# Optimization experiments

Hardware: AMD Instinct MI355X
Metric: run time of the kernel (lower is better)

The kernel has to match this reference:

```python
import jax, jax.numpy as jnp
import numpy as np

N = 100000      # nodes
E = 640000      # directed edges (before self-loops)
F_IN = 128      # num_features
C1 = 64         # latent_size (conv1 out, heads=1)
C2 = 16         # num_classes (conv2 out, heads=1)
NEG_SLOPE = 0.2


def setup_inputs() -> dict:
    key = jax.random.key(0)
    ks = jax.random.split(key, 10)
    s = 0.1
    return {
        "x": jax.random.normal(ks[0], (N, F_IN), jnp.float32),
        "edge_index": jax.random.randint(ks[1], (2, E), 0, N, dtype=jnp.int32),
        "W1": jax.random.normal(ks[2], (F_IN, C1), jnp.float32) * s,
        "att_src1": jax.random.normal(ks[3], (C1,), jnp.float32) * s,
        "att_dst1": jax.random.normal(ks[4], (C1,), jnp.float32) * s,
        "b1": jax.random.normal(ks[5], (C1,), jnp.float32) * s,
        "W2": jax.random.normal(ks[6], (C1, C2), jnp.float32) * s,
        "att_src2": jax.random.normal(ks[7], (C2,), jnp.float32) * s,
        "att_dst2": jax.random.normal(ks[8], (C2,), jnp.float32) * s,
        "b2": jax.random.normal(ks[9], (C2,), jnp.float32) * s,
    }


def gat_layer(x, src, dst, W, a_src, a_dst, b, n_nodes):
    # x: [N, F] -> h: [N, C] (heads=1)
    h = x @ W
    # per-edge attention logits: alpha_j + alpha_i, then leaky_relu
    alpha = jax.nn.leaky_relu((h @ a_src)[src] + (h @ a_dst)[dst], NEG_SLOPE)
    # scatter-softmax over destination-node groups (numerically stable)
    amax = jax.ops.segment_max(alpha, dst, num_segments=n_nodes)
    e = jnp.exp(alpha - amax[dst])
    denom = jax.ops.segment_sum(e, dst, num_segments=n_nodes)
    w = e / (denom[dst] + 1e-16)
    # gather src features, weight, scatter-add to dst
    out = jax.ops.segment_sum(h[src] * w[:, None], dst, num_segments=n_nodes)
    return out + b


def kl_to_std_normal(out):
    # GIB reparameterize: mean = out[:, :ceil(C/2)], std = softplus(out[:, -ceil(C/2):])
    size = (out.shape[-1] + 1) // 2
    mean = out[:, :size]
    std = jax.nn.softplus(out[:, -size:]) + 1e-10
    kl = -jnp.log(std) + 0.5 * (std * std + mean * mean - 1.0)
    return kl.reshape(out.shape[0], -1, 1)  # [N, size, heads=1]


def reference(x, edge_index, W1, att_src1, att_dst1, b1, W2, att_src2, att_dst2, b2):
    n = x.shape[0]
    loop = jnp.arange(n, dtype=edge_index.dtype)  # PyG GATConv add_self_loops=True
    src = jnp.concatenate([edge_index[0], loop])
    dst = jnp.concatenate([edge_index[1], loop])

    out1 = gat_layer(x, src, dst, W1, att_src1, att_dst1, b1, n)
    ixz1 = kl_to_std_normal(out1)

    h = jax.nn.elu(out1)  # dropout is a no-op in eval mode
    out2 = gat_layer(h, src, dst, W2, att_src2, att_dst2, b2, n)
    ixz2 = kl_to_std_normal(out2)

    return (out2, ixz1, ixz2)
```

## Files before the change

kernel.cpp:

```cpp
#include <hip/hip_runtime.h>
#include <math.h>

#define NN 100000
#define NE 640000
#define FIN 128
#define C1 64
#define C2 16
#define NEG_SLOPE 0.2f
#define SLOTS 32
#define G1_BLOCKS ((NN + 127) / 128)
#define SORT_EPB 2048
#define SORT_NBLK ((NE + SORT_EPB - 1) / SORT_EPB)
#define NBUCK 512
#define NBUCK_USED ((NN + 255) / 256)

typedef unsigned int uint32;
typedef __attribute__((ext_vector_type(8))) short bf16x8;
typedef __attribute__((ext_vector_type(4))) float f32x4;

static __device__ __forceinline__ float lrelu(float x) { return x > 0.f ? x : NEG_SLOPE * x; }
static __device__ __forceinline__ float softplusn(float x) {
    return fmaxf(x, 0.f) + __logf(1.f + __expf(-fabsf(x)));
}
static __device__ __forceinline__ unsigned short f2bf(float f) {
    uint32 u = __float_as_uint(f);
    u += 0x7fffu + ((u >> 16) & 1u);
    return (unsigned short)(u >> 16);
}
static __device__ __forceinline__ float bf2f_lo(uint32 p) { return __uint_as_float(p << 16); }
static __device__ __forceinline__ float bf2f_hi(uint32 p) { return __uint_as_float(p & 0xffff0000u); }

#define G1T 2
__global__ __launch_bounds__(256, 3) void k_g1hist(
        const float* __restrict__ x, const float* __restrict__ W1,
        const float* __restrict__ attS, const float* __restrict__ attD,
        unsigned short* __restrict__ h1b, float* __restrict__ as1, float* __restrict__ ad1,
        const int* __restrict__ ei, int* __restrict__ blockHist) {
    __shared__ uint32 ts[4][16][36];
    __shared__ int lh[NBUCK];
    if (blockIdx.x >= G1_BLOCKS) {
        int blk = (int)blockIdx.x - G1_BLOCKS;
        int t = threadIdx.x;
        for (int i = t; i < NBUCK; i += 256) lh[i] = 0;
        __syncthreads();
        int base = blk * SORT_EPB;
#pragma unroll
        for (int k = 0; k < 8; k++) {
            int e = base + k * 256 + t;
            if (e < NE) atomicAdd(&lh[ei[NE + e] >> 8], 1);
        }
        __syncthreads();
        for (int i = t; i < NBUCK; i += 256) blockHist[i * SORT_NBLK + blk] = lh[i];
        return;
    }
    int lane = threadIdx.x & 63;
    int wv = threadIdx.x >> 6;
    int col = lane & 15;
    int g = lane >> 4;
    int wbase = (blockIdx.x * 4 + wv) * (G1T * 16);
    if (wbase >= NN) return;

    bf16x8 bfr[4][4];
#pragma unroll
    for (int t = 0; t < 4; t++)
#pragma unroll
        for (int j = 0; j < 4; j++) {
            int c = col + j * 16;
#pragma unroll
            for (int i = 0; i < 8; i++)
                bfr[t][j][i] = (short)f2bf(W1[(t * 32 + g * 8 + i) * C1 + c]);
        }
    float ats[4], atd[4];
#pragma unroll
    for (int j = 0; j < 4; j++) { ats[j] = attS[col + j * 16]; atd[j] = attD[col + j * 16]; }

    for (int tl = 0; tl < G1T; tl++) {
        int tbase = wbase + tl * 16;
        int arow = tbase + col; if (arow > NN - 1) arow = NN - 1;
        const float* xr = &x[(size_t)arow * FIN];
        float4 f0[4], f1[4];
#pragma unroll
        for (int t = 0; t < 4; t++) {
            f0[t] = *reinterpret_cast<const float4*>(&xr[t * 32 + g * 8]);
            f1[t] = *reinterpret_cast<const float4*>(&xr[t * 32 + g * 8 + 4]);
        }
        bf16x8 a[4];
#pragma unroll
        for (int t = 0; t < 4; t++) {
            a[t][0] = (short)f2bf(f0[t].x); a[t][1] = (short)f2bf(f0[t].y);
            a[t][2] = (short)f2bf(f0[t].z); a[t][3] = (short)f2bf(f0[t].w);
            a[t][4] = (short)f2bf(f1[t].x); a[t][5] = (short)f2bf(f1[t].y);
            a[t][6] = (short)f2bf(f1[t].z); a[t][7] = (short)f2bf(f1[t].w);
        }
        f32x4 acc[4];
#pragma unroll
        for (int j = 0; j < 4; j++) acc[j] = (f32x4){0.f, 0.f, 0.f, 0.f};
#pragma unroll
        for (int t = 0; t < 4; t++)
#pragma unroll
            for (int j = 0; j < 4; j++)
                acc[j] = __builtin_amdgcn_mfma_f32_16x16x32_bf16(a[t], bfr[t][j], acc[j], 0, 0, 0);

        float sA[4] = {0.f, 0.f, 0.f, 0.f}, sD[4] = {0.f, 0.f, 0.f, 0.f};
        unsigned short* tsw = (unsigned short*)&ts[wv][0][0];
#pragma unroll
        for (int reg = 0; reg < 4; reg++) {
            int trow = g * 4 + reg;
#pragma unroll
            for (int j = 0; j < 4; j++) {
                float v = acc[j][reg];
                tsw[trow * 72 + col + j * 16] = f2bf(v);
                sA[reg] = fmaf(v, ats[j], sA[reg]);
                sD[reg] = fmaf(v, atd[j], sD[reg]);
            }
        }
        __builtin_amdgcn_wave_barrier();
        {
            int rrow = lane >> 2, rq = lane & 3;
            uint4 w0 = *reinterpret_cast<const uint4*>(&ts[wv][rrow][rq * 8]);
            uint4 w1 = *reinterpret_cast<const uint4*>(&ts[wv][rrow][rq * 8 + 4]);
            int orow = tbase + rrow;
            if (orow < NN) {
                unsigned short* op = &h1b[(size_t)orow * C1 + rq * 16];
                *reinterpret_cast<uint4*>(op) = w0;
                *reinterpret_cast<uint4*>(op + 8) = w1;
            }
        }
        __builtin_amdgcn_wave_barrier();
#pragma unroll
        for (int off = 8; off; off >>= 1)
#pragma unroll
            for (int reg = 0; reg < 4; reg++) {
                sA[reg] += __shfl_xor(sA[reg], off);
                sD[reg] += __shfl_xor(sD[reg], off);
            }
        if (col == 0) {
#pragma unroll
            for (int reg = 0; reg < 4; reg++) {
                int row = tbase + g * 4 + reg;
                if (row < NN) { as1[row] = sA[reg]; ad1[row] = sD[reg]; }
            }
        }
    }
}

__global__ __launch_bounds__(256) void k_scan(int* __restrict__ blockHist, int* __restrict__ bucketCnt) {
    __shared__ int s[SORT_NBLK];
    int b = blockIdx.x, t = threadIdx.x;
    for (int i = t; i < SORT_NBLK; i += 256) s[i] = blockHist[b * SORT_NBLK + i];
    __syncthreads();
    for (int d = 1; d < SORT_NBLK; d <<= 1) {
        int i0 = t, i1 = t + 256;
        int v0 = 0, v1 = 0;
        if (i0 >= d && i0 < SORT_NBLK) v0 = s[i0 - d];
        if (i1 >= d && i1 < SORT_NBLK) v1 = s[i1 - d];
        __syncthreads();
        if (i0 >= d && i0 < SORT_NBLK) s[i0] += v0;
        if (i1 >= d && i1 < SORT_NBLK) s[i1] += v1;
        __syncthreads();
    }
    for (int i = t; i < SORT_NBLK; i += 256)
        blockHist[b * SORT_NBLK + i] = (i == 0) ? 0 : s[i - 1];
    if (t == 0) bucketCnt[b] = s[SORT_NBLK - 1];
}

__global__ __launch_bounds__(256) void k_scat1(const int* __restrict__ ei,
        const int* __restrict__ blockHist, uint32* __restrict__ ebuf) {
    __shared__ int lh[NBUCK];
    int t = threadIdx.x;
    for (int i = t; i < NBUCK; i += 256) lh[i] = blockHist[i * SORT_NBLK + blockIdx.x];
    __syncthreads();
    int base = blockIdx.x * SORT_EPB;
#pragma unroll
    for (int k = 0; k < 8; k++) {
        int e = base + k * 256 + t;
        if (e < NE) {
            int src = ei[e], dst = ei[NE + e];
            int bin = dst >> 8;
            int pos = atomicAdd(&lh[bin], 1);
            ebuf[bin * SORT_EPB + pos] = ((uint32)src << 8) | (uint32)(dst & 255);
        }
    }
}

__global__ __launch_bounds__(256, 4) void k_agg1(
        const uint32* __restrict__ ebuf, const int* __restrict__ bucketCnt,
        const float* __restrict__ as1, const float* __restrict__ ad1,
        const unsigned short* __restrict__ h1b, const float* __restrict__ b1,
        unsigned short* __restrict__ heb, float* __restrict__ ixz1) {
    __shared__ int lcnt[256];
    __shared__ int lcsr[256 * SLOTS];
    int t = threadIdx.x, b = blockIdx.x;
    lcnt[t] = 0;
    for (int i = t; i < 256 * SLOTS; i += 256) lcsr[i] = 0;
    __syncthreads();
    int n = bucketCnt[b]; if (n > SORT_EPB) n = SORT_EPB;
    for (int i = t; i < n; i += 256) {
        uint32 e = ebuf[b * SORT_EPB + i];
        int ln = (int)(e & 255u);
        int pos = atomicAdd(&lcnt[ln], 1);
        if (pos < SLOTS) lcsr[ln * SLOTS + pos] = (int)(e >> 8);
    }
    __syncthreads();
    int lane = t & 63, wv = t >> 6;
    int grp = lane >> 4, gl = lane & 15;
    int gbase = grp << 4;
    for (int it = 0; it < 16; it++) {
        int ln = it * 16 + wv * 4 + grp;
        int node = b * 256 + ln;
        if (node >= NN) continue;
        int dcnt = lcnt[ln];
        int s_l = lcsr[ln * SLOTS + gl];
        int4 S0 = *reinterpret_cast<const int4*>(&lcsr[ln * SLOTS]);
        int4 S1 = *reinterpret_cast<const int4*>(&lcsr[ln * SLOTS + 4]);
        int4 S2 = *reinterpret_cast<const int4*>(&lcsr[ln * SLOTS + 8]);
        int4 S3 = *reinterpret_cast<const int4*>(&lcsr[ln * SLOTS + 12]);
        float adn = ad1[node];
        float asn = as1[node];
        float asv = as1[s_l];
        float4 o;
        if (dcnt <= 16) {
            float al = (gl < dcnt) ? lrelu(asv + adn) : -1e30f;
            float wl = __expf(al);
            float den = wl;
#pragma unroll
            for (int off = 8; off; off >>= 1) den += __shfl_xor(den, off);
            float wself = __expf(lrelu(asn + adn));
            den += wself;
            float inv = __builtin_amdgcn_rcpf(den + 1e-16f);
            wl *= inv; wself *= inv;
            const unsigned short* hb = h1b + gl * 4;
            uint2 PS  = *reinterpret_cast<const uint2*>(&hb[(size_t)node * C1]);
            uint2 P0  = *reinterpret_cast<const uint2*>(&hb[(size_t)S0.x * C1]);
            uint2 P1  = *reinterpret_cast<const uint2*>(&hb[(size_t)S0.y * C1]);
            uint2 P2  = *reinterpret_cast<const uint2*>(&hb[(size_t)S0.z * C1]);
            uint2 P3  = *reinterpret_cast<const uint2*>(&hb[(size_t)S0.w * C1]);
            uint2 P4  = *reinterpret_cast<const uint2*>(&hb[(size_t)S1.x * C1]);
            uint2 P5  = *reinterpret_cast<const uint2*>(&hb[(size_t)S1.y * C1]);
            uint2 P6  = *reinterpret_cast<const uint2*>(&hb[(size_t)S1.z * C1]);
            uint2 P7  = *reinterpret_cast<const uint2*>(&hb[(size_t)S1.w * C1]);
            uint2 P8  = *reinterpret_cast<const uint2*>(&hb[(size_t)S2.x * C1]);
            uint2 P9  = *reinterpret_cast<const uint2*>(&hb[(size_t)S2.y * C1]);
            uint2 P10 = *reinterpret_cast<const uint2*>(&hb[(size_t)S2.z * C1]);
            uint2 P11 = *reinterpret_cast<const uint2*>(&hb[(size_t)S2.w * C1]);
            uint2 P12 = *reinterpret_cast<const uint2*>(&hb[(size_t)S3.x * C1]);
            uint2 P13 = *reinterpret_cast<const uint2*>(&hb[(size_t)S3.y * C1]);
            uint2 P14 = *reinterpret_cast<const uint2*>(&hb[(size_t)S3.z * C1]);
            uint2 P15 = *reinterpret_cast<const uint2*>(&hb[(size_t)S3.w * C1]);
            float4 acc;
            acc.x = wself * bf2f_lo(PS.x);
            acc.y = wself * bf2f_hi(PS.x);
            acc.z = wself * bf2f_lo(PS.y);
            acc.w = wself * bf2f_hi(PS.y);
#define ACC1(k, Pk) { float w = __shfl(wl, gbase | k); \
            acc.x = fmaf(w, bf2f_lo(Pk.x), acc.x); acc.y = fmaf(w, bf2f_hi(Pk.x), acc.y); \
            acc.z = fmaf(w, bf2f_lo(Pk.y), acc.z); acc.w = fmaf(w, bf2f_hi(Pk.y), acc.w); }
            ACC1(0, P0)  ACC1(1, P1)  ACC1(2, P2)  ACC1(3, P3)
            ACC1(4, P4)  ACC1(5, P5)  ACC1(6, P6)  ACC1(7, P7)
            ACC1(8, P8)  ACC1(9, P9)  ACC1(10, P10) ACC1(11, P11)
            ACC1(12, P12) ACC1(13, P13) ACC1(14, P14) ACC1(15, P15)
#undef ACC1
            o = acc;
        } else {
            int dcl = dcnt < SLOTS ? dcnt : SLOTS;
            float aself = lrelu(asn + adn);
            float m = aself;
            for (int e = gl; e < dcl; e += 16) m = fmaxf(m, lrelu(as1[lcsr[ln * SLOTS + e]] + adn));
#pragma unroll
            for (int off = 8; off; off >>= 1) m = fmaxf(m, __shfl_xor(m, off));
            float den = 0.f;
            for (int e = gl; e < dcl; e += 16) den += __expf(lrelu(as1[lcsr[ln * SLOTS + e]] + adn) - m);
#pragma unroll
            for (int off = 8; off; off >>= 1) den += __shfl_xor(den, off);
            den += __expf(aself - m);
            float inv = __builtin_amdgcn_rcpf(den + 1e-16f);
            float wsf = __expf(aself - m) * inv;
            uint2 ps = *reinterpret_cast<const uint2*>(&h1b[(size_t)node * C1 + gl * 4]);
            float4 acc;
            acc.x = wsf * bf2f_lo(ps.x);
            acc.y = wsf * bf2f_hi(ps.x);
            acc.z = wsf * bf2f_lo(ps.y);
            acc.w = wsf * bf2f_hi(ps.y);
            for (int e = 0; e < dcl; e++) {
                int s = lcsr[ln * SLOTS + e];
                float wgt = __expf(lrelu(as1[s] + adn) - m) * inv;
                uint2 p = *reinterpret_cast<const uint2*>(&h1b[(size_t)s * C1 + gl * 4]);
                acc.x = fmaf(wgt, bf2f_lo(p.x), acc.x);
                acc.y = fmaf(wgt, bf2f_hi(p.x), acc.y);
                acc.z = fmaf(wgt, bf2f_lo(p.y), acc.z);
                acc.w = fmaf(wgt, bf2f_hi(p.y), acc.w);
            }
            o = acc;
        }
        float4 bv = *reinterpret_cast<const float4*>(&b1[gl * 4]);
        o.x += bv.x; o.y += bv.y; o.z += bv.z; o.w += bv.w;
        float4 he;
        he.x = o.x > 0.f ? o.x : __expf(o.x) - 1.f;
        he.y = o.y > 0.f ? o.y : __expf(o.y) - 1.f;
        he.z = o.z > 0.f ? o.z : __expf(o.z) - 1.f;
        he.w = o.w > 0.f ? o.w : __expf(o.w) - 1.f;
        uint2 hw;
        hw.x = (uint32)f2bf(he.x) | ((uint32)f2bf(he.y) << 16);
        hw.y = (uint32)f2bf(he.z) | ((uint32)f2bf(he.w) << 16);
        *reinterpret_cast<uint2*>(&heb[(size_t)node * C1 + gl * 4]) = hw;
        float4 oth;
        oth.x = __shfl_down(o.x, 8);
        oth.y = __shfl_down(o.y, 8);
        oth.z = __shfl_down(o.z, 8);
        oth.w = __shfl_down(o.w, 8);
        if (gl < 8) {
            float4 kl; float sd;
            sd = softplusn(oth.x) + 1e-10f; kl.x = -__logf(sd) + 0.5f * (sd * sd + o.x * o.x - 1.f);
            sd = softplusn(oth.y) + 1e-10f; kl.y = -__logf(sd) + 0.5f * (sd * sd + o.y * o.y - 1.f);
            sd = softplusn(oth.z) + 1e-10f; kl.z = -__logf(sd) + 0.5f * (sd * sd + o.z * o.z - 1.f);
            sd = softplusn(oth.w) + 1e-10f; kl.w = -__logf(sd) + 0.5f * (sd * sd + o.w * o.w - 1.f);
            *reinterpret_cast<float4*>(&ixz1[(size_t)node * 32 + gl * 4]) = kl;
        }
    }
}

#define G2T 4
__global__ __launch_bounds__(256, 4) void k_gemm2(
        const unsigned short* __restrict__ heb, const float* __restrict__ W2,
        const float* __restrict__ attS, const float* __restrict__ attD,
        unsigned short* __restrict__ h2b, float* __restrict__ as2, float* __restrict__ ad2) {
    int lane = threadIdx.x & 63;
    int wv = threadIdx.x >> 6;
    int col = lane & 15, g = lane >> 4;
    int wbase = (blockIdx.x * 4 + wv) * (G2T * 16);
    if (wbase >= NN) return;
    bf16x8 bfr[2];
#pragma unroll
    for (int t = 0; t < 2; t++)
#pragma unroll
        for (int i = 0; i < 8; i++)
            bfr[t][i] = (short)f2bf(W2[(t * 32 + g * 8 + i) * C2 + col]);
    float ats = attS[col], atd = attD[col];
#pragma unroll
    for (int tl = 0; tl < G2T; tl++) {
        int tbase = wbase + tl * 16;
        if (tbase >= NN) break;
        int arow = tbase + col; if (arow > NN - 1) arow = NN - 1;
        bf16x8 a0 = *reinterpret_cast<const bf16x8*>(&heb[(size_t)arow * C1 + g * 8]);
        bf16x8 a1 = *reinterpret_cast<const bf16x8*>(&heb[(size_t)arow * C1 + 32 + g * 8]);
        f32x4 acc = (f32x4){0.f, 0.f, 0.f, 0.f};
        acc = __builtin_amdgcn_mfma_f32_16x16x32_bf16(a0, bfr[0], acc, 0, 0, 0);
        acc = __builtin_amdgcn_mfma_f32_16x16x32_bf16(a1, bfr[1], acc, 0, 0, 0);
        float sA[4], sD[4];
#pragma unroll
        for (int reg = 0; reg < 4; reg++) {
            int row = tbase + g * 4 + reg;
            if (row < NN) h2b[(size_t)row * C2 + col] = f2bf(acc[reg]);
            sA[reg] = acc[reg] * ats;
            sD[reg] = acc[reg] * atd;
        }
#pragma unroll
        for (int off = 8; off; off >>= 1)
#pragma unroll
            for (int reg = 0; reg < 4; reg++) {
                sA[reg] += __shfl_xor(sA[reg], off);
                sD[reg] += __shfl_xor(sD[reg], off);
            }
        if (col == 0) {
#pragma unroll
            for (int reg = 0; reg < 4; reg++) {
                int row = tbase + g * 4 + reg;
                if (row < NN) { as2[row] = sA[reg]; ad2[row] = sD[reg]; }
            }
        }
    }
}

__global__ __launch_bounds__(256, 4) void k_agg2(
        const uint32* __restrict__ ebuf, const int* __restrict__ bucketCnt,
        const float* __restrict__ as2, const float* __restrict__ ad2,
        const unsigned short* __restrict__ h2b, const float* __restrict__ b2,
        float* __restrict__ out2, float* __restrict__ ixz2) {
    __shared__ int lcnt[256];
    __shared__ int lcsr[256 * SLOTS];
    int t = threadIdx.x, b = blockIdx.x;
    lcnt[t] = 0;
    for (int i = t; i < 256 * SLOTS; i += 256) lcsr[i] = 0;
    __syncthreads();
    int n = bucketCnt[b]; if (n > SORT_EPB) n = SORT_EPB;
    for (int i = t; i < n; i += 256) {
        uint32 e = ebuf[b * SORT_EPB + i];
        int ln = (int)(e & 255u);
        int pos = atomicAdd(&lcnt[ln], 1);
        if (pos < SLOTS) lcsr[ln * SLOTS + pos] = (int)(e >> 8);
    }
    __syncthreads();
    int lane = t & 63, wv = t >> 6;
    int grp = lane >> 4, gl = lane & 15;
    int gbase = grp << 4;
    int f4 = gl & 3, eg = gl >> 2;
    for (int it = 0; it < 16; it++) {
        int ln = it * 16 + wv * 4 + grp;
        int node = b * 256 + ln;
        if (node >= NN) continue;
        int dcnt = lcnt[ln];
        int s_l = lcsr[ln * SLOTS + gl];
        int sk0 = lcsr[ln * SLOTS + eg];
        int sk1 = lcsr[ln * SLOTS + 4 + eg];
        int sk2 = lcsr[ln * SLOTS + 8 + eg];
        int sk3 = lcsr[ln * SLOTS + 12 + eg];
        float adn = ad2[node];
        float asn = as2[node];
        float asv = as2[s_l];
        float out;
        if (dcnt <= 16) {
            float al = (gl < dcnt) ? lrelu(asv + adn) : -1e30f;
            float wl = __expf(al);
            float den = wl;
#pragma unroll
            for (int off = 8; off; off >>= 1) den += __shfl_xor(den, off);
            float wself = __expf(lrelu(asn + adn));
            den += wself;
            float inv = __builtin_amdgcn_rcpf(den + 1e-16f);
            wl *= inv; wself *= inv;
            uint2 PS = *reinterpret_cast<const uint2*>(&h2b[(size_t)node * C2 + f4 * 4]);
            uint2 P0 = *reinterpret_cast<const uint2*>(&h2b[(size_t)sk0 * C2 + f4 * 4]);
            uint2 P1 = *reinterpret_cast<const uint2*>(&h2b[(size_t)sk1 * C2 + f4 * 4]);
            uint2 P2 = *reinterpret_cast<const uint2*>(&h2b[(size_t)sk2 * C2 + f4 * 4]);
            uint2 P3 = *reinterpret_cast<const uint2*>(&h2b[(size_t)sk3 * C2 + f4 * 4]);
            float ws = (eg == 0) ? wself : 0.f;
            float4 acc;
            acc.x = ws * bf2f_lo(PS.x);
            acc.y = ws * bf2f_hi(PS.x);
            acc.z = ws * bf2f_lo(PS.y);
            acc.w = ws * bf2f_hi(PS.y);
            float w0 = __shfl(wl, gbase | eg);
            float w1 = __shfl(wl, gbase | (4 + eg));
            float w2 = __shfl(wl, gbase | (8 + eg));
            float w3 = __shfl(wl, gbase | (12 + eg));
            acc.x = fmaf(w0, bf2f_lo(P0.x), acc.x);
            acc.y = fmaf(w0, bf2f_hi(P0.x), acc.y);
            acc.z = fmaf(w0, bf2f_lo(P0.y), acc.z);
            acc.w = fmaf(w0, bf2f_hi(P0.y), acc.w);
            acc.x = fmaf(w1, bf2f_lo(P1.x), acc.x);
            acc.y = fmaf(w1, bf2f_hi(P1.x), acc.y);
            acc.z = fmaf(w1, bf2f_lo(P1.y), acc.z);
            acc.w = fmaf(w1, bf2f_hi(P1.y), acc.w);
            acc.x = fmaf(w2, bf2f_lo(P2.x), acc.x);
            acc.y = fmaf(w2, bf2f_hi(P2.x), acc.y);
            acc.z = fmaf(w2, bf2f_lo(P2.y), acc.z);
            acc.w = fmaf(w2, bf2f_hi(P2.y), acc.w);
            acc.x = fmaf(w3, bf2f_lo(P3.x), acc.x);
            acc.y = fmaf(w3, bf2f_hi(P3.x), acc.y);
            acc.z = fmaf(w3, bf2f_lo(P3.y), acc.z);
            acc.w = fmaf(w3, bf2f_hi(P3.y), acc.w);
#pragma unroll
            for (int off = 4; off <= 8; off <<= 1) {
                acc.x += __shfl_xor(acc.x, off);
                acc.y += __shfl_xor(acc.y, off);
                acc.z += __shfl_xor(acc.z, off);
                acc.w += __shfl_xor(acc.w, off);
            }
            int srcl = gbase | (gl >> 2);
            float t0 = __shfl(acc.x, srcl);
            float t1 = __shfl(acc.y, srcl);
            float t2 = __shfl(acc.z, srcl);
            float t3 = __shfl(acc.w, srcl);
            float t01 = (gl & 1) ? t1 : t0;
            float t23 = (gl & 1) ? t3 : t2;
            out = (gl & 2) ? t23 : t01;
        } else {
            int dcl = dcnt < SLOTS ? dcnt : SLOTS;
            float aself = lrelu(asn + adn);
            float m = aself;
            for (int e = gl; e < dcl; e += 16) m = fmaxf(m, lrelu(as2[lcsr[ln * SLOTS + e]] + adn));
#pragma unroll
            for (int off = 8; off; off >>= 1) m = fmaxf(m, __shfl_xor(m, off));
            float den = 0.f;
            for (int e = gl; e < dcl; e += 16) den += __expf(lrelu(as2[lcsr[ln * SLOTS + e]] + adn) - m);
#pragma unroll
            for (int off = 8; off; off >>= 1) den += __shfl_xor(den, off);
            den += __expf(aself - m);
            float inv = __builtin_amdgcn_rcpf(den + 1e-16f);
            float wsf = __expf(aself - m) * inv;
            float acc = wsf * __uint_as_float(((uint32)h2b[(size_t)node * C2 + gl]) << 16);
            for (int e = 0; e < dcl; e++) {
                int s = lcsr[ln * SLOTS + e];
                float wgt = __expf(lrelu(as2[s] + adn) - m) * inv;
                acc = fmaf(wgt, __uint_as_float(((uint32)h2b[(size_t)s * C2 + gl]) << 16), acc);
            }
            out = acc;
        }
        out += b2[gl];
        out2[(size_t)node * C2 + gl] = out;
        float other = __shfl_down(out, 8);
        if (gl < 8) {
            float sd = softplusn(other) + 1e-10f;
            float kl = -__logf(sd) + 0.5f * (sd * sd + out * out - 1.f);
            ixz2[(size_t)node * 8 + gl] = kl;
        }
    }
}

extern "C" void kernel_launch(void* const* d_in, const int* in_sizes, int n_in,
                              void* d_out, int out_size, void* d_ws, size_t ws_size,
                              hipStream_t stream) {
    const float* x     = (const float*)d_in[0];
    const int*   ei    = (const int*)d_in[1];
    const float* W1    = (const float*)d_in[2];
    const float* aS1   = (const float*)d_in[3];
    const float* aD1   = (const float*)d_in[4];
    const float* b1    = (const float*)d_in[5];
    const float* W2    = (const float*)d_in[6];
    const float* aS2   = (const float*)d_in[7];
    const float* aD2   = (const float*)d_in[8];
    const float* b2    = (const float*)d_in[9];

    float* out = (float*)d_out;
    float* out2 = out;
    float* ixz1 = out + (size_t)NN * C2;
    float* ixz2 = ixz1 + (size_t)NN * 32;

    char* p = (char*)d_ws;
    auto alloc = [&](size_t bytes) -> void* {
        void* r = (void*)p;
        p += (bytes + 255) & ~(size_t)255;
        return r;
    };
    int* blockHist  = (int*)alloc((size_t)NBUCK * SORT_NBLK * 4);
    int* bucketCnt  = (int*)alloc((size_t)NBUCK * 4);
    uint32* ebuf    = (uint32*)alloc((size_t)NBUCK * SORT_EPB * 4);
    unsigned short* h1b = (unsigned short*)alloc((size_t)NN * C1 * 2);
    float* as1   = (float*)alloc((size_t)NN * 4);
    float* ad1   = (float*)alloc((size_t)NN * 4);
    unsigned short* heb = (unsigned short*)alloc((size_t)NN * C1 * 2);
    unsigned short* h2b = (unsigned short*)alloc((size_t)NN * C2 * 2);
    float* as2   = (float*)alloc((size_t)NN * 4);
    float* ad2   = (float*)alloc((size_t)NN * 4);
    (void)ws_size; (void)in_sizes; (void)n_in; (void)out_size;

    k_g1hist<<<G1_BLOCKS + SORT_NBLK, 256, 0, stream>>>(x, W1, aS1, aD1, h1b, as1, ad1, ei, blockHist);

    k_scan <<<NBUCK, 256, 0, stream>>>(blockHist, bucketCnt);
    k_scat1<<<SORT_NBLK, 256, 0, stream>>>(ei, blockHist, ebuf);

    k_agg1<<<NBUCK_USED, 256, 0, stream>>>(ebuf, bucketCnt, as1, ad1, h1b, b1, heb, ixz1);

    k_gemm2<<<(NN + 4 * G2T * 16 - 1) / (4 * G2T * 16), 256, 0, stream>>>(heb, W2, aS2, aD2, h2b, as2, ad2);
    k_agg2<<<NBUCK_USED, 256, 0, stream>>>(ebuf, bucketCnt, as2, ad2, h2b, b2, out2, ixz2);
}
```

Measured before the change: 117.2 us.

## Shrink destination bins to 16 nodes so aggregation launches one block per bin

```diff
diff --git a/kernel.cpp b/kernel.cpp
--- a/kernel.cpp
+++ b/kernel.cpp
@@ -11,8 +11,8 @@
 #define G1_BLOCKS ((NN + 127) / 128)
 #define SORT_EPB 2048
 #define SORT_NBLK ((NE + SORT_EPB - 1) / SORT_EPB)
-#define NBUCK 512
-#define NBUCK_USED ((NN + 255) / 256)
+#define NBIN ((NN + 15) / 16)
+#define BINCAP 192
 
 typedef unsigned int uint32;
 typedef __attribute__((ext_vector_type(8))) short bf16x8;
@@ -37,20 +37,20 @@
         unsigned short* __restrict__ h1b, float* __restrict__ as1, float* __restrict__ ad1,
         const int* __restrict__ ei, int* __restrict__ blockHist) {
     __shared__ uint32 ts[4][16][36];
-    __shared__ int lh[NBUCK];
+    __shared__ int lh[NBIN];
     if (blockIdx.x >= G1_BLOCKS) {
         int blk = (int)blockIdx.x - G1_BLOCKS;
         int t = threadIdx.x;
-        for (int i = t; i < NBUCK; i += 256) lh[i] = 0;
+        for (int i = t; i < NBIN; i += 256) lh[i] = 0;
         __syncthreads();
         int base = blk * SORT_EPB;
 #pragma unroll
         for (int k = 0; k < 8; k++) {
             int e = base + k * 256 + t;
-            if (e < NE) atomicAdd(&lh[ei[NE + e] >> 8], 1);
+            if (e < NE) atomicAdd(&lh[ei[NE + e] >> 4], 1);
         }
         __syncthreads();
-        for (int i = t; i < NBUCK; i += 256) blockHist[i * SORT_NBLK + blk] = lh[i];
+        for (int i = t; i < NBIN; i += 256) blockHist[(size_t)i * SORT_NBLK + blk] = lh[i];
         return;
     }
     int lane = threadIdx.x & 63;
@@ -144,10 +144,10 @@
     }
 }
 
-__global__ __launch_bounds__(256) void k_scan(int* __restrict__ blockHist, int* __restrict__ bucketCnt) {
+__global__ __launch_bounds__(256) void k_scan(int* __restrict__ blockHist, int* __restrict__ binCnt) {
     __shared__ int s[SORT_NBLK];
     int b = blockIdx.x, t = threadIdx.x;
-    for (int i = t; i < SORT_NBLK; i += 256) s[i] = blockHist[b * SORT_NBLK + i];
+    for (int i = t; i < SORT_NBLK; i += 256) s[i] = blockHist[(size_t)b * SORT_NBLK + i];
     __syncthreads();
     for (int d = 1; d < SORT_NBLK; d <<= 1) {
         int i0 = t, i1 = t + 256;
@@ -160,15 +160,15 @@
         __syncthreads();
     }
     for (int i = t; i < SORT_NBLK; i += 256)
-        blockHist[b * SORT_NBLK + i] = (i == 0) ? 0 : s[i - 1];
-    if (t == 0) bucketCnt[b] = s[SORT_NBLK - 1];
+        blockHist[(size_t)b * SORT_NBLK + i] = (i == 0) ? 0 : s[i - 1];
+    if (t == 0) binCnt[b] = s[SORT_NBLK - 1];
 }
 
 __global__ __launch_bounds__(256) void k_scat1(const int* __restrict__ ei,
         const int* __restrict__ blockHist, uint32* __restrict__ ebuf) {
-    __shared__ int lh[NBUCK];
+    __shared__ int lh[NBIN];
     int t = threadIdx.x;
-    for (int i = t; i < NBUCK; i += 256) lh[i] = blockHist[i * SORT_NBLK + blockIdx.x];
+    for (int i = t; i < NBIN; i += 256) lh[i] = blockHist[(size_t)i * SORT_NBLK + blockIdx.x];
     __syncthreads();
     int base = blockIdx.x * SORT_EPB;
 #pragma unroll
@@ -176,146 +176,145 @@
         int e = base + k * 256 + t;
         if (e < NE) {
             int src = ei[e], dst = ei[NE + e];
-            int bin = dst >> 8;
+            int bin = dst >> 4;
             int pos = atomicAdd(&lh[bin], 1);
-            ebuf[bin * SORT_EPB + pos] = ((uint32)src << 8) | (uint32)(dst & 255);
+            if (pos < BINCAP)
+                ebuf[(size_t)bin * BINCAP + pos] = ((uint32)src << 4) | (uint32)(dst & 15);
         }
     }
 }
 
 __global__ __launch_bounds__(256, 4) void k_agg1(
-        const uint32* __restrict__ ebuf, const int* __restrict__ bucketCnt,
+        const uint32* __restrict__ ebuf, const int* __restrict__ binCnt,
         const float* __restrict__ as1, const float* __restrict__ ad1,
         const unsigned short* __restrict__ h1b, const float* __restrict__ b1,
         unsigned short* __restrict__ heb, float* __restrict__ ixz1) {
-    __shared__ int lcnt[256];
-    __shared__ int lcsr[256 * SLOTS];
+    __shared__ int lcnt[16];
+    __shared__ int lcsr[16 * SLOTS];
     int t = threadIdx.x, b = blockIdx.x;
-    lcnt[t] = 0;
-    for (int i = t; i < 256 * SLOTS; i += 256) lcsr[i] = 0;
+    if (t < 16) lcnt[t] = 0;
+    for (int i = t; i < 16 * SLOTS; i += 256) lcsr[i] = 0;
     __syncthreads();
-    int n = bucketCnt[b]; if (n > SORT_EPB) n = SORT_EPB;
-    for (int i = t; i < n; i += 256) {
-        uint32 e = ebuf[b * SORT_EPB + i];
-        int ln = (int)(e & 255u);
+    int n = binCnt[b]; if (n > BINCAP) n = BINCAP;
+    if (t < n) {
+        uint32 e = ebuf[(size_t)b * BINCAP + t];
+        int ln = (int)(e & 15u);
         int pos = atomicAdd(&lcnt[ln], 1);
-        if (pos < SLOTS) lcsr[ln * SLOTS + pos] = (int)(e >> 8);
+        if (pos < SLOTS) lcsr[ln * SLOTS + pos] = (int)(e >> 4);
     }
     __syncthreads();
     int lane = t & 63, wv = t >> 6;
     int grp = lane >> 4, gl = lane & 15;
     int gbase = grp << 4;
-    for (int it = 0; it < 16; it++) {
-        int ln = it * 16 + wv * 4 + grp;
-        int node = b * 256 + ln;
-        if (node >= NN) continue;
-        int dcnt = lcnt[ln];
-        int s_l = lcsr[ln * SLOTS + gl];
-        int4 S0 = *reinterpret_cast<const int4*>(&lcsr[ln * SLOTS]);
-        int4 S1 = *reinterpret_cast<const int4*>(&lcsr[ln * SLOTS + 4]);
-        int4 S2 = *reinterpret_cast<const int4*>(&lcsr[ln * SLOTS + 8]);
-        int4 S3 = *reinterpret_cast<const int4*>(&lcsr[ln * SLOTS + 12]);
-        float adn = ad1[node];
-        float asn = as1[node];
-        float asv = as1[s_l];
-        float4 o;
-        if (dcnt <= 16) {
-            float al = (gl < dcnt) ? lrelu(asv + adn) : -1e30f;
-            float wl = __expf(al);
-            float den = wl;
-#pragma unroll
-            for (int off = 8; off; off >>= 1) den += __shfl_xor(den, off);
-            float wself = __expf(lrelu(asn + adn));
-            den += wself;
-            float inv = __builtin_amdgcn_rcpf(den + 1e-16f);
-            wl *= inv; wself *= inv;
-            const unsigned short* hb = h1b + gl * 4;
-            uint2 PS  = *reinterpret_cast<const uint2*>(&hb[(size_t)node * C1]);
-            uint2 P0  = *reinterpret_cast<const uint2*>(&hb[(size_t)S0.x * C1]);
-            uint2 P1  = *reinterpret_cast<const uint2*>(&hb[(size_t)S0.y * C1]);
-            uint2 P2  = *reinterpret_cast<const uint2*>(&hb[(size_t)S0.z * C1]);
-            uint2 P3  = *reinterpret_cast<const uint2*>(&hb[(size_t)S0.w * C1]);
-            uint2 P4  = *reinterpret_cast<const uint2*>(&hb[(size_t)S1.x * C1]);
-            uint2 P5  = *reinterpret_cast<const uint2*>(&hb[(size_t)S1.y * C1]);
-            uint2 P6  = *reinterpret_cast<const uint2*>(&hb[(size_t)S1.z * C1]);
-            uint2 P7  = *reinterpret_cast<const uint2*>(&hb[(size_t)S1.w * C1]);
-            uint2 P8  = *reinterpret_cast<const uint2*>(&hb[(size_t)S2.x * C1]);
-            uint2 P9  = *reinterpret_cast<const uint2*>(&hb[(size_t)S2.y * C1]);
-            uint2 P10 = *reinterpret_cast<const uint2*>(&hb[(size_t)S2.z * C1]);
-            uint2 P11 = *reinterpret_cast<const uint2*>(&hb[(size_t)S2.w * C1]);
-            uint2 P12 = *reinterpret_cast<const uint2*>(&hb[(size_t)S3.x * C1]);
-            uint2 P13 = *reinterpret_cast<const uint2*>(&hb[(size_t)S3.y * C1]);
-            uint2 P14 = *reinterpret_cast<const uint2*>(&hb[(size_t)S3.z * C1]);
-            uint2 P15 = *reinterpret_cast<const uint2*>(&hb[(size_t)S3.w * C1]);
-            float4 acc;
-            acc.x = wself * bf2f_lo(PS.x);
-            acc.y = wself * bf2f_hi(PS.x);
-            acc.z = wself * bf2f_lo(PS.y);
-            acc.w = wself * bf2f_hi(PS.y);
+    int ln = wv * 4 + grp;
+    int node = b * 16 + ln;
+    if (node >= NN) return;
+    int dcnt = lcnt[ln];
+    int s_l = lcsr[ln * SLOTS + gl];
+    int4 S0 = *reinterpret_cast<const int4*>(&lcsr[ln * SLOTS]);
+    int4 S1 = *reinterpret_cast<const int4*>(&lcsr[ln * SLOTS + 4]);
+    int4 S2 = *reinterpret_cast<const int4*>(&lcsr[ln * SLOTS + 8]);
+    int4 S3 = *reinterpret_cast<const int4*>(&lcsr[ln * SLOTS + 12]);
+    float adn = ad1[node];
+    float asn = as1[node];
+    float asv = as1[s_l];
+    float4 o;
+    if (dcnt <= 16) {
+        float al = (gl < dcnt) ? lrelu(asv + adn) : -1e30f;
+        float wl = __expf(al);
+        float den = wl;
+#pragma unroll
+        for (int off = 8; off; off >>= 1) den += __shfl_xor(den, off);
+        float wself = __expf(lrelu(asn + adn));
+        den += wself;
+        float inv = __builtin_amdgcn_rcpf(den + 1e-16f);
+        wl *= inv; wself *= inv;
+        const unsigned short* hb = h1b + gl * 4;
+        uint2 PS  = *reinterpret_cast<const uint2*>(&hb[(size_t)node * C1]);
+        uint2 P0  = *reinterpret_cast<const uint2*>(&hb[(size_t)S0.x * C1]);
+        uint2 P1  = *reinterpret_cast<const uint2*>(&hb[(size_t)S0.y * C1]);
+        uint2 P2  = *reinterpret_cast<const uint2*>(&hb[(size_t)S0.z * C1]);
+        uint2 P3  = *reinterpret_cast<const uint2*>(&hb[(size_t)S0.w * C1]);
+        uint2 P4  = *reinterpret_cast<const uint2*>(&hb[(size_t)S1.x * C1]);
+        uint2 P5  = *reinterpret_cast<const uint2*>(&hb[(size_t)S1.y * C1]);
+        uint2 P6  = *reinterpret_cast<const uint2*>(&hb[(size_t)S1.z * C1]);
+        uint2 P7  = *reinterpret_cast<const uint2*>(&hb[(size_t)S1.w * C1]);
+        uint2 P8  = *reinterpret_cast<const uint2*>(&hb[(size_t)S2.x * C1]);
+        uint2 P9  = *reinterpret_cast<const uint2*>(&hb[(size_t)S2.y * C1]);
+        uint2 P10 = *reinterpret_cast<const uint2*>(&hb[(size_t)S2.z * C1]);
+        uint2 P11 = *reinterpret_cast<const uint2*>(&hb[(size_t)S2.w * C1]);
+        uint2 P12 = *reinterpret_cast<const uint2*>(&hb[(size_t)S3.x * C1]);
+        uint2 P13 = *reinterpret_cast<const uint2*>(&hb[(size_t)S3.y * C1]);
+        uint2 P14 = *reinterpret_cast<const uint2*>(&hb[(size_t)S3.z * C1]);
+        uint2 P15 = *reinterpret_cast<const uint2*>(&hb[(size_t)S3.w * C1]);
+        float4 acc;
+        acc.x = wself * bf2f_lo(PS.x);
+        acc.y = wself * bf2f_hi(PS.x);
+        acc.z = wself * bf2f_lo(PS.y);
+        acc.w = wself * bf2f_hi(PS.y);
 #define ACC1(k, Pk) { float w = __shfl(wl, gbase | k); \
-            acc.x = fmaf(w, bf2f_lo(Pk.x), acc.x); acc.y = fmaf(w, bf2f_hi(Pk.x), acc.y); \
-            acc.z = fmaf(w, bf2f_lo(Pk.y), acc.z); acc.w = fmaf(w, bf2f_hi(Pk.y), acc.w); }
-            ACC1(0, P0)  ACC1(1, P1)  ACC1(2, P2)  ACC1(3, P3)
-            ACC1(4, P4)  ACC1(5, P5)  ACC1(6, P6)  ACC1(7, P7)
-            ACC1(8, P8)  ACC1(9, P9)  ACC1(10, P10) ACC1(11, P11)
-            ACC1(12, P12) ACC1(13, P13) ACC1(14, P14) ACC1(15, P15)
+        acc.x = fmaf(w, bf2f_lo(Pk.x), acc.x); acc.y = fmaf(w, bf2f_hi(Pk.x), acc.y); \
+        acc.z = fmaf(w, bf2f_lo(Pk.y), acc.z); acc.w = fmaf(w, bf2f_hi(Pk.y), acc.w); }
+        ACC1(0, P0)  ACC1(1, P1)  ACC1(2, P2)  ACC1(3, P3)
+        ACC1(4, P4)  ACC1(5, P5)  ACC1(6, P6)  ACC1(7, P7)
+        ACC1(8, P8)  ACC1(9, P9)  ACC1(10, P10) ACC1(11, P11)
+        ACC1(12, P12) ACC1(13, P13) ACC1(14, P14) ACC1(15, P15)
 #undef ACC1
-            o = acc;
-        } else {
-            int dcl = dcnt < SLOTS ? dcnt : SLOTS;
-            float aself = lrelu(asn + adn);
-            float m = aself;
-            for (int e = gl; e < dcl; e += 16) m = fmaxf(m, lrelu(as1[lcsr[ln * SLOTS + e]] + adn));
-#pragma unroll
-            for (int off = 8; off; off >>= 1) m = fmaxf(m, __shfl_xor(m, off));
-            float den = 0.f;
-            for (int e = gl; e < dcl; e += 16) den += __expf(lrelu(as1[lcsr[ln * SLOTS + e]] + adn) - m);
-#pragma unroll
-            for (int off = 8; off; off >>= 1) den += __shfl_xor(den, off);
-            den += __expf(aself - m);
-            float inv = __builtin_amdgcn_rcpf(den + 1e-16f);
-            float wsf = __expf(aself - m) * inv;
-            uint2 ps = *reinterpret_cast<const uint2*>(&h1b[(size_t)node * C1 + gl * 4]);
-            float4 acc;
-            acc.x = wsf * bf2f_lo(ps.x);
-            acc.y = wsf * bf2f_hi(ps.x);
-            acc.z = wsf * bf2f_lo(ps.y);
-            acc.w = wsf * bf2f_hi(ps.y);
-            for (int e = 0; e < dcl; e++) {
-                int s = lcsr[ln * SLOTS + e];
-                float wgt = __expf(lrelu(as1[s] + adn) - m) * inv;
-                uint2 p = *reinterpret_cast<const uint2*>(&h1b[(size_t)s * C1 + gl * 4]);
-                acc.x = fmaf(wgt, bf2f_lo(p.x), acc.x);
-                acc.y = fmaf(wgt, bf2f_hi(p.x), acc.y);
-                acc.z = fmaf(wgt, bf2f_lo(p.y), acc.z);
-                acc.w = fmaf(wgt, bf2f_hi(p.y), acc.w);
-            }
-            o = acc;
-        }
-        float4 bv = *reinterpret_cast<const float4*>(&b1[gl * 4]);
-        o.x += bv.x; o.y += bv.y; o.z += bv.z; o.w += bv.w;
-        float4 he;
-        he.x = o.x > 0.f ? o.x : __expf(o.x) - 1.f;
-        he.y = o.y > 0.f ? o.y : __expf(o.y) - 1.f;
-        he.z = o.z > 0.f ? o.z : __expf(o.z) - 1.f;
-        he.w = o.w > 0.f ? o.w : __expf(o.w) - 1.f;
-        uint2 hw;
-        hw.x = (uint32)f2bf(he.x) | ((uint32)f2bf(he.y) << 16);
-        hw.y = (uint32)f2bf(he.z) | ((uint32)f2bf(he.w) << 16);
-        *reinterpret_cast<uint2*>(&heb[(size_t)node * C1 + gl * 4]) = hw;
-        float4 oth;
-        oth.x = __shfl_down(o.x, 8);
-        oth.y = __shfl_down(o.y, 8);
-        oth.z = __shfl_down(o.z, 8);
-        oth.w = __shfl_down(o.w, 8);
-        if (gl < 8) {
-            float4 kl; float sd;
-            sd = softplusn(oth.x) + 1e-10f; kl.x = -__logf(sd) + 0.5f * (sd * sd + o.x * o.x - 1.f);
-            sd = softplusn(oth.y) + 1e-10f; kl.y = -__logf(sd) + 0.5f * (sd * sd + o.y * o.y - 1.f);
-            sd = softplusn(oth.z) + 1e-10f; kl.z = -__logf(sd) + 0.5f * (sd * sd + o.z * o.z - 1.f);
-            sd = softplusn(oth.w) + 1e-10f; kl.w = -__logf(sd) + 0.5f * (sd * sd + o.w * o.w - 1.f);
-            *reinterpret_cast<float4*>(&ixz1[(size_t)node * 32 + gl * 4]) = kl;
-        }
+        o = acc;
+    } else {
+        int dcl = dcnt < SLOTS ? dcnt : SLOTS;
+        float aself = lrelu(asn + adn);
+        float m = aself;
+        for (int e = gl; e < dcl; e += 16) m = fmaxf(m, lrelu(as1[lcsr[ln * SLOTS + e]] + adn));
+#pragma unroll
+        for (int off = 8; off; off >>= 1) m = fmaxf(m, __shfl_xor(m, off));
+        float den = 0.f;
+        for (int e = gl; e < dcl; e += 16) den += __expf(lrelu(as1[lcsr[ln * SLOTS + e]] + adn) - m);
+#pragma unroll
+        for (int off = 8; off; off >>= 1) den += __shfl_xor(den, off);
+        den += __expf(aself - m);
+        float inv = __builtin_amdgcn_rcpf(den + 1e-16f);
+        float wsf = __expf(aself - m) * inv;
+        uint2 ps = *reinterpret_cast<const uint2*>(&h1b[(size_t)node * C1 + gl * 4]);
+        float4 acc;
+        acc.x = wsf * bf2f_lo(ps.x);
+        acc.y = wsf * bf2f_hi(ps.x);
+        acc.z = wsf * bf2f_lo(ps.y);
+        acc.w = wsf * bf2f_hi(ps.y);
+        for (int e = 0; e < dcl; e++) {
+            int s = lcsr[ln * SLOTS + e];
+            float wgt = __expf(lrelu(as1[s] + adn) - m) * inv;
+            uint2 p = *reinterpret_cast<const uint2*>(&h1b[(size_t)s * C1 + gl * 4]);
+            acc.x = fmaf(wgt, bf2f_lo(p.x), acc.x);
+            acc.y = fmaf(wgt, bf2f_hi(p.x), acc.y);
+            acc.z = fmaf(wgt, bf2f_lo(p.y), acc.z);
+            acc.w = fmaf(wgt, bf2f_hi(p.y), acc.w);
+        }
+        o = acc;
+    }
+    float4 bv = *reinterpret_cast<const float4*>(&b1[gl * 4]);
+    o.x += bv.x; o.y += bv.y; o.z += bv.z; o.w += bv.w;
+    float4 he;
+    he.x = o.x > 0.f ? o.x : __expf(o.x) - 1.f;
+    he.y = o.y > 0.f ? o.y : __expf(o.y) - 1.f;
+    he.z = o.z > 0.f ? o.z : __expf(o.z) - 1.f;
+    he.w = o.w > 0.f ? o.w : __expf(o.w) - 1.f;
+    uint2 hw;
+    hw.x = (uint32)f2bf(he.x) | ((uint32)f2bf(he.y) << 16);
+    hw.y = (uint32)f2bf(he.z) | ((uint32)f2bf(he.w) << 16);
+    *reinterpret_cast<uint2*>(&heb[(size_t)node * C1 + gl * 4]) = hw;
+    float4 oth;
+    oth.x = __shfl_down(o.x, 8);
+    oth.y = __shfl_down(o.y, 8);
+    oth.z = __shfl_down(o.z, 8);
+    oth.w = __shfl_down(o.w, 8);
+    if (gl < 8) {
+        float4 kl; float sd;
+        sd = softplusn(oth.x) + 1e-10f; kl.x = -__logf(sd) + 0.5f * (sd * sd + o.x * o.x - 1.f);
+        sd = softplusn(oth.y) + 1e-10f; kl.y = -__logf(sd) + 0.5f * (sd * sd + o.y * o.y - 1.f);
+        sd = softplusn(oth.z) + 1e-10f; kl.z = -__logf(sd) + 0.5f * (sd * sd + o.z * o.z - 1.f);
+        sd = softplusn(oth.w) + 1e-10f; kl.w = -__logf(sd) + 0.5f * (sd * sd + o.w * o.w - 1.f);
+        *reinterpret_cast<float4*>(&ixz1[(size_t)node * 32 + gl * 4]) = kl;
     }
 }
 
@@ -372,128 +371,126 @@
 }
 
 __global__ __launch_bounds__(256, 4) void k_agg2(
-        const uint32* __restrict__ ebuf, const int* __restrict__ bucketCnt,
+        const uint32* __restrict__ ebuf, const int* __restrict__ binCnt,
         const float* __restrict__ as2, const float* __restrict__ ad2,
         const unsigned short* __restrict__ h2b, const float* __restrict__ b2,
         float* __restrict__ out2, float* __restrict__ ixz2) {
-    __shared__ int lcnt[256];
-    __shared__ int lcsr[256 * SLOTS];
+    __shared__ int lcnt[16];
+    __shared__ int lcsr[16 * SLOTS];
     int t = threadIdx.x, b = blockIdx.x;
-    lcnt[t] = 0;
-    for (int i = t; i < 256 * SLOTS; i += 256) lcsr[i] = 0;
+    if (t < 16) lcnt[t] = 0;
+    for (int i = t; i < 16 * SLOTS; i += 256) lcsr[i] = 0;
     __syncthreads();
-    int n = bucketCnt[b]; if (n > SORT_EPB) n = SORT_EPB;
-    for (int i = t; i < n; i += 256) {
-        uint32 e = ebuf[b * SORT_EPB + i];
-        int ln = (int)(e & 255u);
+    int n = binCnt[b]; if (n > BINCAP) n = BINCAP;
+    if (t < n) {
+        uint32 e = ebuf[(size_t)b * BINCAP + t];
+        int ln = (int)(e & 15u);
         int pos = atomicAdd(&lcnt[ln], 1);
-        if (pos < SLOTS) lcsr[ln * SLOTS + pos] = (int)(e >> 8);
+        if (pos < SLOTS) lcsr[ln * SLOTS + pos] = (int)(e >> 4);
     }
     __syncthreads();
     int lane = t & 63, wv = t >> 6;
     int grp = lane >> 4, gl = lane & 15;
     int gbase = grp << 4;
     int f4 = gl & 3, eg = gl >> 2;
-    for (int it = 0; it < 16; it++) {
-        int ln = it * 16 + wv * 4 + grp;
-        int node = b * 256 + ln;
-        if (node >= NN) continue;
-        int dcnt = lcnt[ln];
-        int s_l = lcsr[ln * SLOTS + gl];
-        int sk0 = lcsr[ln * SLOTS + eg];
-        int sk1 = lcsr[ln * SLOTS + 4 + eg];
-        int sk2 = lcsr[ln * SLOTS + 8 + eg];
-        int sk3 = lcsr[ln * SLOTS + 12 + eg];
-        float adn = ad2[node];
-        float asn = as2[node];
-        float asv = as2[s_l];
-        float out;
-        if (dcnt <= 16) {
-            float al = (gl < dcnt) ? lrelu(asv + adn) : -1e30f;
-            float wl = __expf(al);
-            float den = wl;
-#pragma unroll
-            for (int off = 8; off; off >>= 1) den += __shfl_xor(den, off);
-            float wself = __expf(lrelu(asn + adn));
-            den += wself;
-            float inv = __builtin_amdgcn_rcpf(den + 1e-16f);
-            wl *= inv; wself *= inv;
-            uint2 PS = *reinterpret_cast<const uint2*>(&h2b[(size_t)node * C2 + f4 * 4]);
-            uint2 P0 = *reinterpret_cast<const uint2*>(&h2b[(size_t)sk0 * C2 + f4 * 4]);
-            uint2 P1 = *reinterpret_cast<const uint2*>(&h2b[(size_t)sk1 * C2 + f4 * 4]);
-            uint2 P2 = *reinterpret_cast<const uint2*>(&h2b[(size_t)sk2 * C2 + f4 * 4]);
-            uint2 P3 = *reinterpret_cast<const uint2*>(&h2b[(size_t)sk3 * C2 + f4 * 4]);
-            float ws = (eg == 0) ? wself : 0.f;
-            float4 acc;
-            acc.x = ws * bf2f_lo(PS.x);
-            acc.y = ws * bf2f_hi(PS.x);
-            acc.z = ws * bf2f_lo(PS.y);
-            acc.w = ws * bf2f_hi(PS.y);
-            float w0 = __shfl(wl, gbase | eg);
-            float w1 = __shfl(wl, gbase | (4 + eg));
-            float w2 = __shfl(wl, gbase | (8 + eg));
-            float w3 = __shfl(wl, gbase | (12 + eg));
-            acc.x = fmaf(w0, bf2f_lo(P0.x), acc.x);
-            acc.y = fmaf(w0, bf2f_hi(P0.x), acc.y);
-            acc.z = fmaf(w0, bf2f_lo(P0.y), acc.z);
-            acc.w = fmaf(w0, bf2f_hi(P0.y), acc.w);
-            acc.x = fmaf(w1, bf2f_lo(P1.x), acc.x);
-            acc.y = fmaf(w1, bf2f_hi(P1.x), acc.y);
-            acc.z = fmaf(w1, bf2f_lo(P1.y), acc.z);
-            acc.w = fmaf(w1, bf2f_hi(P1.y), acc.w);
-            acc.x = fmaf(w2, bf2f_lo(P2.x), acc.x);
-            acc.y = fmaf(w2, bf2f_hi(P2.x), acc.y);
-            acc.z = fmaf(w2, bf2f_lo(P2.y), acc.z);
-            acc.w = fmaf(w2, bf2f_hi(P2.y), acc.w);
-            acc.x = fmaf(w3, bf2f_lo(P3.x), acc.x);
-            acc.y = fmaf(w3, bf2f_hi(P3.x), acc.y);
-            acc.z = fmaf(w3, bf2f_lo(P3.y), acc.z);
-            acc.w = fmaf(w3, bf2f_hi(P3.y), acc.w);
-#pragma unroll
-            for (int off = 4; off <= 8; off <<= 1) {
-                acc.x += __shfl_xor(acc.x, off);
-                acc.y += __shfl_xor(acc.y, off);
-                acc.z += __shfl_xor(acc.z, off);
-                acc.w += __shfl_xor(acc.w, off);
-            }
-            int srcl = gbase | (gl >> 2);
-            float t0 = __shfl(acc.x, srcl);
-            float t1 = __shfl(acc.y, srcl);
-            float t2 = __shfl(acc.z, srcl);
-            float t3 = __shfl(acc.w, srcl);
-            float t01 = (gl & 1) ? t1 : t0;
-            float t23 = (gl & 1) ? t3 : t2;
-            out = (gl & 2) ? t23 : t01;
-        } else {
-            int dcl = dcnt < SLOTS ? dcnt : SLOTS;
-            float aself = lrelu(asn + adn);
-            float m = aself;
-            for (int e = gl; e < dcl; e += 16) m = fmaxf(m, lrelu(as2[lcsr[ln * SLOTS + e]] + adn));
-#pragma unroll
-            for (int off = 8; off; off >>= 1) m = fmaxf(m, __shfl_xor(m, off));
-            float den = 0.f;
-            for (int e = gl; e < dcl; e += 16) den += __expf(lrelu(as2[lcsr[ln * SLOTS + e]] + adn) - m);
-#pragma unroll
-            for (int off = 8; off; off >>= 1) den += __shfl_xor(den, off);
-            den += __expf(aself - m);
-            float inv = __builtin_amdgcn_rcpf(den + 1e-16f);
-            float wsf = __expf(aself - m) * inv;
-            float acc = wsf * __uint_as_float(((uint32)h2b[(size_t)node * C2 + gl]) << 16);
-            for (int e = 0; e < dcl; e++) {
-                int s = lcsr[ln * SLOTS + e];
-                float wgt = __expf(lrelu(as2[s] + adn) - m) * inv;
-                acc = fmaf(wgt, __uint_as_float(((uint32)h2b[(size_t)s * C2 + gl]) << 16), acc);
-            }
-            out = acc;
-        }
-        out += b2[gl];
-        out2[(size_t)node * C2 + gl] = out;
-        float other = __shfl_down(out, 8);
-        if (gl < 8) {
-            float sd = softplusn(other) + 1e-10f;
-            float kl = -__logf(sd) + 0.5f * (sd * sd + out * out - 1.f);
-            ixz2[(size_t)node * 8 + gl] = kl;
-        }
+    int ln = wv * 4 + grp;
+    int node = b * 16 + ln;
+    if (node >= NN) return;
+    int dcnt = lcnt[ln];
+    int s_l = lcsr[ln * SLOTS + gl];
+    int sk0 = lcsr[ln * SLOTS + eg];
+    int sk1 = lcsr[ln * SLOTS + 4 + eg];
+    int sk2 = lcsr[ln * SLOTS + 8 + eg];
+    int sk3 = lcsr[ln * SLOTS + 12 + eg];
+    float adn = ad2[node];
+    float asn = as2[node];
+    float asv = as2[s_l];
+    float out;
+    if (dcnt <= 16) {
+        float al = (gl < dcnt) ? lrelu(asv + adn) : -1e30f;
+        float wl = __expf(al);
+        float den = wl;
+#pragma unroll
+        for (int off = 8; off; off >>= 1) den += __shfl_xor(den, off);
+        float wself = __expf(lrelu(asn + adn));
+        den += wself;
+        float inv = __builtin_amdgcn_rcpf(den + 1e-16f);
+        wl *= inv; wself *= inv;
+        uint2 PS = *reinterpret_cast<const uint2*>(&h2b[(size_t)node * C2 + f4 * 4]);
+        uint2 P0 = *reinterpret_cast<const uint2*>(&h2b[(size_t)sk0 * C2 + f4 * 4]);
+        uint2 P1 = *reinterpret_cast<const uint2*>(&h2b[(size_t)sk1 * C2 + f4 * 4]);
+        uint2 P2 = *reinterpret_cast<const uint2*>(&h2b[(size_t)sk2 * C2 + f4 * 4]);
+        uint2 P3 = *reinterpret_cast<const uint2*>(&h2b[(size_t)sk3 * C2 + f4 * 4]);
+        float ws = (eg == 0) ? wself : 0.f;
+        float4 acc;
+        acc.x = ws * bf2f_lo(PS.x);
+        acc.y = ws * bf2f_hi(PS.x);
+        acc.z = ws * bf2f_lo(PS.y);
+        acc.w = ws * bf2f_hi(PS.y);
+        float w0 = __shfl(wl, gbase | eg);
+        float w1 = __shfl(wl, gbase | (4 + eg));
+        float w2 = __shfl(wl, gbase | (8 + eg));
+        float w3 = __shfl(wl, gbase | (12 + eg));
+        acc.x = fmaf(w0, bf2f_lo(P0.x), acc.x);
+        acc.y = fmaf(w0, bf2f_hi(P0.x), acc.y);
+        acc.z = fmaf(w0, bf2f_lo(P0.y), acc.z);
+        acc.w = fmaf(w0, bf2f_hi(P0.y), acc.w);
+        acc.x = fmaf(w1, bf2f_lo(P1.x), acc.x);
+        acc.y = fmaf(w1, bf2f_hi(P1.x), acc.y);
+        acc.z = fmaf(w1, bf2f_lo(P1.y), acc.z);
+        acc.w = fmaf(w1, bf2f_hi(P1.y), acc.w);
+        acc.x = fmaf(w2, bf2f_lo(P2.x), acc.x);
+        acc.y = fmaf(w2, bf2f_hi(P2.x), acc.y);
+        acc.z = fmaf(w2, bf2f_lo(P2.y), acc.z);
+        acc.w = fmaf(w2, bf2f_hi(P2.y), acc.w);
+        acc.x = fmaf(w3, bf2f_lo(P3.x), acc.x);
+        acc.y = fmaf(w3, bf2f_hi(P3.x), acc.y);
+        acc.z = fmaf(w3, bf2f_lo(P3.y), acc.z);
+        acc.w = fmaf(w3, bf2f_hi(P3.y), acc.w);
+#pragma unroll
+        for (int off = 4; off <= 8; off <<= 1) {
+            acc.x += __shfl_xor(acc.x, off);
+            acc.y += __shfl_xor(acc.y, off);
+            acc.z += __shfl_xor(acc.z, off);
+            acc.w += __shfl_xor(acc.w, off);
+        }
+        int srcl = gbase | (gl >> 2);
+        float t0 = __shfl(acc.x, srcl);
+        float t1 = __shfl(acc.y, srcl);
+        float t2 = __shfl(acc.z, srcl);
+        float t3 = __shfl(acc.w, srcl);
+        float t01 = (gl & 1) ? t1 : t0;
+        float t23 = (gl & 1) ? t3 : t2;
+        out = (gl & 2) ? t23 : t01;
+    } else {
+        int dcl = dcnt < SLOTS ? dcnt : SLOTS;
+        float aself = lrelu(asn + adn);
+        float m = aself;
+        for (int e = gl; e < dcl; e += 16) m = fmaxf(m, lrelu(as2[lcsr[ln * SLOTS + e]] + adn));
+#pragma unroll
+        for (int off = 8; off; off >>= 1) m = fmaxf(m, __shfl_xor(m, off));
+        float den = 0.f;
+        for (int e = gl; e < dcl; e += 16) den += __expf(lrelu(as2[lcsr[ln * SLOTS + e]] + adn) - m);
+#pragma unroll
+        for (int off = 8; off; off >>= 1) den += __shfl_xor(den, off);
+        den += __expf(aself - m);
+        float inv = __builtin_amdgcn_rcpf(den + 1e-16f);
+        float wsf = __expf(aself - m) * inv;
+        float acc = wsf * __uint_as_float(((uint32)h2b[(size_t)node * C2 + gl]) << 16);
+        for (int e = 0; e < dcl; e++) {
+            int s = lcsr[ln * SLOTS + e];
+            float wgt = __expf(lrelu(as2[s] + adn) - m) * inv;
+            acc = fmaf(wgt, __uint_as_float(((uint32)h2b[(size_t)s * C2 + gl]) << 16), acc);
+        }
+        out = acc;
+    }
+    out += b2[gl];
+    out2[(size_t)node * C2 + gl] = out;
+    float other = __shfl_down(out, 8);
+    if (gl < 8) {
+        float sd = softplusn(other) + 1e-10f;
+        float kl = -__logf(sd) + 0.5f * (sd * sd + out * out - 1.f);
+        ixz2[(size_t)node * 8 + gl] = kl;
     }
 }
 
@@ -522,9 +519,9 @@
         p += (bytes + 255) & ~(size_t)255;
         return r;
     };
-    int* blockHist  = (int*)alloc((size_t)NBUCK * SORT_NBLK * 4);
-    int* bucketCnt  = (int*)alloc((size_t)NBUCK * 4);
-    uint32* ebuf    = (uint32*)alloc((size_t)NBUCK * SORT_EPB * 4);
+    int* blockHist  = (int*)alloc((size_t)NBIN * SORT_NBLK * 4);
+    int* binCnt     = (int*)alloc((size_t)NBIN * 4);
+    uint32* ebuf    = (uint32*)alloc((size_t)NBIN * BINCAP * 4);
     unsigned short* h1b = (unsigned short*)alloc((size_t)NN * C1 * 2);
     float* as1   = (float*)alloc((size_t)NN * 4);
     float* ad1   = (float*)alloc((size_t)NN * 4);
@@ -536,11 +533,11 @@
 
     k_g1hist<<<G1_BLOCKS + SORT_NBLK, 256, 0, stream>>>(x, W1, aS1, aD1, h1b, as1, ad1, ei, blockHist);
 
-    k_scan <<<NBUCK, 256, 0, stream>>>(blockHist, bucketCnt);
+    k_scan <<<NBIN, 256, 0, stream>>>(blockHist, binCnt);
     k_scat1<<<SORT_NBLK, 256, 0, stream>>>(ei, blockHist, ebuf);
 
-    k_agg1<<<NBUCK_USED, 256, 0, stream>>>(ebuf, bucketCnt, as1, ad1, h1b, b1, heb, ixz1);
+    k_agg1<<<NBIN, 256, 0, stream>>>(ebuf, binCnt, as1, ad1, h1b, b1, heb, ixz1);
 
     k_gemm2<<<(NN + 4 * G2T * 16 - 1) / (4 * G2T * 16), 256, 0, stream>>>(heb, W2, aS2, aD2, h2b, as2, ad2);
-    k_agg2<<<NBUCK_USED, 256, 0, stream>>>(ebuf, bucketCnt, as2, ad2, h2b, b2, out2, ixz2);
-}
+    k_agg2<<<NBIN, 256, 0, stream>>>(ebuf, binCnt, as2, ad2, h2b, b2, out2, ixz2);
+}
```

New measurement: 122.4 us. +4.4%, slower.
